# Performance work log

Measured on AMD Instinct MI355X. Metric: run time of the kernel, lower is better.

The kernel has to match this reference:

```python
import math
import jax, jax.numpy as jnp
import numpy as np

B, S, H = 8, 1024, 1024
NH = 16
HD = H // NH  # 64


def setup_inputs() -> dict:
    key = jax.random.key(0)
    k1, k2, k3, k4 = jax.random.split(key, 4)
    hidden_states = jax.random.normal(k1, (B, S, H), dtype=jnp.float32)
    attention_mask = jax.random.randint(k2, (B, 1, 1, S), 0, 2, dtype=jnp.int32)
    w_qkv = jax.random.normal(k3, (H, 3 * H), dtype=jnp.float32) * (1.0 / math.sqrt(H))
    b_qkv = jax.random.normal(k4, (3 * H,), dtype=jnp.float32) * 0.02
    return {"hidden_states": hidden_states, "attention_mask": attention_mask,
            "w_qkv": w_qkv, "b_qkv": b_qkv}


def reference(hidden_states, attention_mask, w_qkv, b_qkv):
    b, s, _ = hidden_states.shape
    # fused QKV projection: [b, s, 3H]
    qkv = jnp.einsum('bsh,hk->bsk', hidden_states, w_qkv) + b_qkv
    # view (b, s, nh, 3*hd) -> permute -> chunk last dim (per-head q|k|v layout)
    qkv = qkv.reshape(b, s, NH, 3, HD)
    qkv = jnp.transpose(qkv, (0, 2, 1, 3, 4))      # [b, nh, s, 3, hd]
    q, k, v = qkv[..., 0, :], qkv[..., 1, :], qkv[..., 2, :]
    # raw scores, then FusedScaleMaskSoftmax semantics: scale * scores, mask, fp32 softmax
    scores = jnp.einsum('bhqd,bhkd->bhqk', q, k)
    scale = math.sqrt(HD)  # module passes sqrt(head_dim) as multiplicative scale
    scores = scores.astype(jnp.float32) * scale
    mask = attention_mask != 0                     # nonzero -> masked (padding)
    scores = jnp.where(mask, jnp.float32(-10000.0), scores)
    probs = jax.nn.softmax(scores, axis=-1).astype(hidden_states.dtype)
    # dropout prob = 0 -> identity
    context = jnp.einsum('bhqk,bhkd->bhqd', probs, v)
    context = jnp.transpose(context, (0, 2, 1, 3)).reshape(b, s, NH * HD)
    return context
```

## Files before the change

### kernel.cpp

```cpp
#include <hip/hip_runtime.h>
#include <math.h>

#define Bdim 8
#define Sdim 1024
#define Hdim 1024
#define NHd 16
#define HDd 64
#define N3H 3072

#define Q_OFF   0u
#define K_OFF   16777216u
#define V_OFF   33554432u
#define WH_OFF  41943040u
#define WL_OFF  45088768u
#define AHI_OFF 0u
#define ALO_OFF 8388608u

typedef __bf16 bf16x8 __attribute__((ext_vector_type(8)));
typedef float  f32x4  __attribute__((ext_vector_type(4)));

__device__ __forceinline__ unsigned short f2bf(float x) {
  unsigned b = __builtin_bit_cast(unsigned, x);
  return (unsigned short)((b + 0x7FFFu + ((b >> 16) & 1u)) >> 16);
}
__device__ __forceinline__ float bf2f(unsigned short h) {
  unsigned b = ((unsigned)h) << 16;
  return __builtin_bit_cast(float, b);
}
__device__ __forceinline__ void split_hl(float v, unsigned short& h, unsigned short& l) {
  h = f2bf(v);
  l = f2bf(v - bf2f(h));
}
__device__ __forceinline__ void async16(void* lds, const void* g) {
  __builtin_amdgcn_global_load_lds((const __attribute__((address_space(1))) unsigned int*)g,
                                   (__attribute__((address_space(3))) unsigned int*)lds, 16, 0, 0);
}

__global__ __launch_bounds__(256) void convert_AW(
    const float* __restrict__ A, const float* __restrict__ W,
    unsigned short* __restrict__ aout, unsigned short* __restrict__ ws)
{
  __shared__ float T[64][65];
  const int tid = threadIdx.x;
  int bid = blockIdx.x;
  if (bid < 4096) {
    size_t i = ((size_t)bid * 256 + tid) * 8;
    float4 a0 = *(const float4*)&A[i];
    float4 a1 = *(const float4*)&A[i + 4];
    float av[8] = {a0.x, a0.y, a0.z, a0.w, a1.x, a1.y, a1.z, a1.w};
    unsigned short h[8], l[8];
    #pragma unroll
    for (int j = 0; j < 8; ++j) split_hl(av[j], h[j], l[j]);
    *(uint4*)&aout[AHI_OFF + i] = *(uint4*)h;
    *(uint4*)&aout[ALO_OFF + i] = *(uint4*)l;
    return;
  }
  bid -= 4096;
  const int n0 = (bid % (N3H / 64)) * 64;
  const int k0 = (bid / (N3H / 64)) * 64;
  #pragma unroll
  for (int r = 0; r < 4; ++r) {
    int k = r * 16 + (tid >> 4);
    int n = (tid & 15) * 4;
    float4 v = *(const float4*)&W[(size_t)(k0 + k) * N3H + n0 + n];
    T[k][n + 0] = v.x; T[k][n + 1] = v.y; T[k][n + 2] = v.z; T[k][n + 3] = v.w;
  }
  __syncthreads();
  int n = tid >> 2;
  int kl = (tid & 3) * 16;
  unsigned short h[16], l[16];
  #pragma unroll
  for (int i = 0; i < 16; ++i) split_hl(T[kl + i][n], h[i], l[i]);
  size_t base = (size_t)(n0 + n) * 1024 + k0 + kl;
  *(uint4*)&ws[WH_OFF + base]     = *(uint4*)&h[0];
  *(uint4*)&ws[WH_OFF + base + 8] = *(uint4*)&h[8];
  *(uint4*)&ws[WL_OFF + base]     = *(uint4*)&l[0];
  *(uint4*)&ws[WL_OFF + base + 8] = *(uint4*)&l[8];
}

__global__ __launch_bounds__(256, 2) void qkv_mfma(
    const unsigned short* __restrict__ ao,
    const unsigned short* __restrict__ ws,
    const float* __restrict__ bias,
    unsigned short* __restrict__ wso)
{
  __shared__ unsigned short sA[2][128 * 32];
  __shared__ unsigned short sB[2][128 * 32];

  const int tid  = threadIdx.x;
  const int wave = tid >> 6;
  const int lane = tid & 63;
  const int l16  = lane & 15;
  const int quad = lane >> 4;

  const int n0 = blockIdx.x * 128;
  const int m0 = blockIdx.y * 128;
  const int wm = (wave >> 1) * 64;
  const int wn = (wave & 1) * 64;

  const unsigned short* Ah = ao + AHI_OFF;
  const unsigned short* Al = ao + ALO_OFF;
  const unsigned short* Wh = ws + WH_OFF;
  const unsigned short* Wl = ws + WL_OFF;

  f32x4 acc[4][4];
  #pragma unroll
  for (int i = 0; i < 4; ++i)
    #pragma unroll
    for (int j = 0; j < 4; ++j) acc[i][j] = (f32x4){0.f, 0.f, 0.f, 0.f};

  for (int kt = 0; kt < 1024; kt += 32) {
    __syncthreads();
    #pragma unroll
    for (int r = 0; r < 2; ++r) {
      int chunk = r * 256 + tid;
      int row = chunk >> 2;
      int c8  = (chunk & 3) << 3;
      int ldsoff = (r * 256 + wave * 64) * 8;
      async16(&sA[0][ldsoff], &Ah[(size_t)(m0 + row) * 1024 + kt + c8]);
      async16(&sA[1][ldsoff], &Al[(size_t)(m0 + row) * 1024 + kt + c8]);
      async16(&sB[0][ldsoff], &Wh[(size_t)(n0 + row) * 1024 + kt + c8]);
      async16(&sB[1][ldsoff], &Wl[(size_t)(n0 + row) * 1024 + kt + c8]);
    }
    __syncthreads();

    bf16x8 af[4][2], bf[4][2];
    #pragma unroll
    for (int i = 0; i < 4; ++i) {
      int row = wm + i * 16 + l16;
      af[i][0] = *(const bf16x8*)&sA[0][row * 32 + quad * 8];
      af[i][1] = *(const bf16x8*)&sA[1][row * 32 + quad * 8];
    }
    #pragma unroll
    for (int j = 0; j < 4; ++j) {
      int row = wn + j * 16 + l16;
      bf[j][0] = *(const bf16x8*)&sB[0][row * 32 + quad * 8];
      bf[j][1] = *(const bf16x8*)&sB[1][row * 32 + quad * 8];
    }
    #pragma unroll
    for (int i = 0; i < 4; ++i)
      #pragma unroll
      for (int j = 0; j < 4; ++j) {
        acc[i][j] = __builtin_amdgcn_mfma_f32_16x16x32_bf16(af[i][0], bf[j][0], acc[i][j], 0, 0, 0);
        acc[i][j] = __builtin_amdgcn_mfma_f32_16x16x32_bf16(af[i][1], bf[j][0], acc[i][j], 0, 0, 0);
        acc[i][j] = __builtin_amdgcn_mfma_f32_16x16x32_bf16(af[i][0], bf[j][1], acc[i][j], 0, 0, 0);
      }
  }

  const int ncol0 = n0 + wn;
  const int which = (ncol0 >> 6) % 3;
  const int head  = ncol0 / 192;
  const int mrow0 = m0 + wm;
  const int bb = mrow0 >> 10;
  const int sb = mrow0 & 1023;
  const int bh = bb * NHd + head;

  float bs[4];
  #pragma unroll
  for (int j = 0; j < 4; ++j) bs[j] = bias[ncol0 + j * 16 + l16];

  if (which == 0) {
    unsigned short* dst = wso + Q_OFF + ((size_t)bh * Sdim + sb) * 128;
    #pragma unroll
    for (int i = 0; i < 4; ++i)
      #pragma unroll
      for (int j = 0; j < 4; ++j) {
        int d = j * 16 + l16;
        #pragma unroll
        for (int r = 0; r < 4; ++r) {
          int s = i * 16 + quad * 4 + r;
          unsigned short h, l;
          split_hl(acc[i][j][r] + bs[j], h, l);
          dst[(size_t)s * 128 + d]      = h;
          dst[(size_t)s * 128 + 64 + d] = l;
        }
      }
  } else if (which == 1) {
    unsigned short* dst = wso + K_OFF + (size_t)bh * 131072 + (size_t)(sb >> 6) * 8192;
    #pragma unroll
    for (int i = 0; i < 4; ++i)
      #pragma unroll
      for (int j = 0; j < 4; ++j) {
        int c = j * 16 + l16;
        #pragma unroll
        for (int r = 0; r < 4; ++r) {
          int sp = i * 16 + quad * 4 + r;
          int idx = ((((sp >> 4) * 4 + (c >> 5)) * 64 + ((c >> 3) & 3) * 16 + (sp & 15)) << 3) + (c & 7);
          unsigned short h, l;
          split_hl(acc[i][j][r] + bs[j], h, l);
          dst[idx]        = h;
          dst[idx + 1024] = l;
        }
      }
  } else {
    unsigned short* dst = wso + V_OFF + (size_t)bh * 65536 + (size_t)(sb >> 6) * 4096;
    #pragma unroll
    for (int i = 0; i < 4; ++i)
      #pragma unroll
      for (int j = 0; j < 4; ++j) {
        int dr = j * 16 + l16;
        int ky = i * 16 + quad * 4;
        int idx = ((((dr >> 4) * 2 + (ky >> 5)) * 64 + ((ky >> 3) & 3) * 16 + (dr & 15)) << 3) + (ky & 7);
        unsigned short p[4];
        #pragma unroll
        for (int r = 0; r < 4; ++r) p[r] = f2bf(acc[i][j][r] + bs[j]);
        *(uint2*)&dst[idx] = *(uint2*)p;
      }
  }
}

__global__ __launch_bounds__(256, 4) void attn_mfma(
    const unsigned short* __restrict__ qhl,
    const unsigned short* __restrict__ khl,
    const unsigned short* __restrict__ vt,
    const int* __restrict__ mask,
    float* __restrict__ out)
{
  __shared__ unsigned short Ks[8192];
  __shared__ unsigned short Vs[4096];
  __shared__ unsigned short Pw[4][1024];
  __shared__ float msks[1024];

  const int tid  = threadIdx.x;
  const int wave = tid >> 6;
  const int lane = tid & 63;
  const int l16  = lane & 15;
  const int quad = lane >> 4;

  const int bh = blockIdx.x & 127;
  const int qt = blockIdx.x >> 7;
  const int bb = bh >> 4;
  const int q0 = qt * 64;

  const unsigned short* kplane = khl + (size_t)bh * 131072;
  const unsigned short* vplane = vt  + (size_t)bh * 65536;

  {
    int4 mv = *(const int4*)&mask[bb * Sdim + tid * 4];
    msks[tid * 4 + 0] = mv.x ? 1.f : 0.f;
    msks[tid * 4 + 1] = mv.y ? 1.f : 0.f;
    msks[tid * 4 + 2] = mv.z ? 1.f : 0.f;
    msks[tid * 4 + 3] = mv.w ? 1.f : 0.f;
  }

  bf16x8 qf[4];
  {
    int row = q0 + wave * 16 + l16;
    const unsigned short* src = qhl + ((size_t)bh * Sdim + row) * 128;
    #pragma unroll
    for (int kk = 0; kk < 4; ++kk)
      qf[kk] = *(const bf16x8*)&src[kk * 32 + quad * 8];
  }

  f32x4 O[4] = {{0.f,0.f,0.f,0.f},{0.f,0.f,0.f,0.f},{0.f,0.f,0.f,0.f},{0.f,0.f,0.f,0.f}};
  float mrow[4] = {-INFINITY, -INFINITY, -INFINITY, -INFINITY};
  float lrow[4] = {0.f, 0.f, 0.f, 0.f};

  #pragma unroll 1
  for (int kt = 0; kt < 16; ++kt) {
    __syncthreads();
    {
      const unsigned short* ksrc = kplane + (size_t)kt * 8192;
      const unsigned short* vsrc = vplane + (size_t)kt * 4096;
      #pragma unroll
      for (int r = 0; r < 4; ++r)
        async16(&Ks[(r * 256 + tid) * 8], &ksrc[(size_t)(r * 256 + tid) * 8]);
      #pragma unroll
      for (int r = 0; r < 2; ++r)
        async16(&Vs[(r * 256 + tid) * 8], &vsrc[(size_t)(r * 256 + tid) * 8]);
    }
    __syncthreads();

    f32x4 sc[4];
    #pragma unroll
    for (int ns = 0; ns < 4; ++ns) {
      f32x4 c = {0.f, 0.f, 0.f, 0.f};
      bf16x8 kf0 = *(const bf16x8*)&Ks[((ns * 4 + 0) * 64 + lane) * 8];
      bf16x8 kf1 = *(const bf16x8*)&Ks[((ns * 4 + 1) * 64 + lane) * 8];
      bf16x8 kf2 = *(const bf16x8*)&Ks[((ns * 4 + 2) * 64 + lane) * 8];
      bf16x8 kf3 = *(const bf16x8*)&Ks[((ns * 4 + 3) * 64 + lane) * 8];
      c = __builtin_amdgcn_mfma_f32_16x16x32_bf16(qf[0], kf0, c, 0, 0, 0);
      c = __builtin_amdgcn_mfma_f32_16x16x32_bf16(qf[1], kf1, c, 0, 0, 0);
      c = __builtin_amdgcn_mfma_f32_16x16x32_bf16(qf[2], kf0, c, 0, 0, 0);
      c = __builtin_amdgcn_mfma_f32_16x16x32_bf16(qf[3], kf1, c, 0, 0, 0);
      c = __builtin_amdgcn_mfma_f32_16x16x32_bf16(qf[0], kf2, c, 0, 0, 0);
      c = __builtin_amdgcn_mfma_f32_16x16x32_bf16(qf[1], kf3, c, 0, 0, 0);
      sc[ns] = c;
    }

    float rmax[4] = {-INFINITY, -INFINITY, -INFINITY, -INFINITY};
    #pragma unroll
    for (int ns = 0; ns < 4; ++ns) {
      float mk = msks[kt * 64 + ns * 16 + l16];
      #pragma unroll
      for (int r = 0; r < 4; ++r) {
        float s = (mk != 0.f) ? -10000.f : sc[ns][r] * 8.f;
        sc[ns][r] = s;
        rmax[r] = fmaxf(rmax[r], s);
      }
    }
    #pragma unroll
    for (int r = 0; r < 4; ++r) {
      float v = rmax[r];
      v = fmaxf(v, __shfl_xor(v, 1, 16));
      v = fmaxf(v, __shfl_xor(v, 2, 16));
      v = fmaxf(v, __shfl_xor(v, 4, 16));
      v = fmaxf(v, __shfl_xor(v, 8, 16));
      rmax[r] = v;
    }

    float alpha[4];
    #pragma unroll
    for (int r = 0; r < 4; ++r) {
      float mn = fmaxf(mrow[r], rmax[r]);
      alpha[r] = __expf(mrow[r] - mn);
      mrow[r] = mn;
      lrow[r] *= alpha[r];
    }
    #pragma unroll
    for (int d = 0; d < 4; ++d)
      #pragma unroll
      for (int r = 0; r < 4; ++r) O[d][r] *= alpha[r];

    float rsum[4] = {0.f, 0.f, 0.f, 0.f};
    #pragma unroll
    for (int ns = 0; ns < 4; ++ns) {
      int key = ns * 16 + l16;
      int cbase = (((key >> 5) * 4 + ((key >> 3) & 3)) * 16 + quad * 4) * 8 + (key & 7);
      #pragma unroll
      for (int r = 0; r < 4; ++r) {
        float p = __expf(sc[ns][r] - mrow[r]);
        rsum[r] += p;
        Pw[wave][cbase + r * 8] = f2bf(p);
      }
    }
    #pragma unroll
    for (int r = 0; r < 4; ++r) {
      float v = rsum[r];
      v += __shfl_xor(v, 1, 16);
      v += __shfl_xor(v, 2, 16);
      v += __shfl_xor(v, 4, 16);
      v += __shfl_xor(v, 8, 16);
      lrow[r] += v;
    }

    bf16x8 pf[2];
    #pragma unroll
    for (int kk = 0; kk < 2; ++kk)
      pf[kk] = *(const bf16x8*)&Pw[wave][((kk * 4 + quad) * 16 + l16) * 8];
    #pragma unroll
    for (int d = 0; d < 4; ++d)
      #pragma unroll
      for (int kk = 0; kk < 2; ++kk) {
        bf16x8 vf = *(const bf16x8*)&Vs[((d * 2 + kk) * 64 + lane) * 8];
        O[d] = __builtin_amdgcn_mfma_f32_16x16x32_bf16(pf[kk], vf, O[d], 0, 0, 0);
      }
  }

  const int h = bh & 15;
  #pragma unroll
  for (int r = 0; r < 4; ++r) {
    float inv = 1.f / lrow[r];
    int q = q0 + wave * 16 + quad * 4 + r;
    float* dst = out + ((size_t)bb * Sdim + q) * Hdim + h * HDd;
    #pragma unroll
    for (int d = 0; d < 4; ++d)
      dst[d * 16 + l16] = O[d][r] * inv;
  }
}

extern "C" void kernel_launch(void* const* d_in, const int* in_sizes, int n_in,
                              void* d_out, int out_size, void* d_ws, size_t ws_size,
                              hipStream_t stream) {
  const float* hs   = (const float*)d_in[0];
  const int*   mask = (const int*)d_in[1];
  const float* w    = (const float*)d_in[2];
  const float* bias = (const float*)d_in[3];
  float* out = (float*)d_out;
  unsigned short* ws = (unsigned short*)d_ws;
  unsigned short* ao = (unsigned short*)d_out;

  convert_AW<<<4096 + (N3H / 64) * (1024 / 64), 256, 0, stream>>>(hs, w, ao, ws);

  qkv_mfma<<<dim3(N3H / 128, 8192 / 128), 256, 0, stream>>>(ao, ws, bias, ws);

  attn_mfma<<<Bdim * NHd * (Sdim / 64), 256, 0, stream>>>(
      ws + Q_OFF, ws + K_OFF, ws + V_OFF, mask, out);
}
```

Measured before the change: 373.9 us.

## Restructure QKV GEMM into 256x192 double-buffered tiles with swizzled LDS

```diff
diff --git a/kernel.cpp b/kernel.cpp
--- a/kernel.cpp
+++ b/kernel.cpp
@@ -78,14 +78,14 @@
   *(uint4*)&ws[WL_OFF + base + 8] = *(uint4*)&l[8];
 }
 
-__global__ __launch_bounds__(256, 2) void qkv_mfma(
+__global__ __launch_bounds__(512, 2) void qkv_mfma(
     const unsigned short* __restrict__ ao,
     const unsigned short* __restrict__ ws,
     const float* __restrict__ bias,
     unsigned short* __restrict__ wso)
 {
-  __shared__ unsigned short sA[2][128 * 32];
-  __shared__ unsigned short sB[2][128 * 32];
+  __shared__ __align__(16) unsigned short sA[2][256 * 64];
+  __shared__ __align__(16) unsigned short sB[2][192 * 64];
 
   const int tid  = threadIdx.x;
   const int wave = tid >> 6;
@@ -93,120 +93,178 @@
   const int l16  = lane & 15;
   const int quad = lane >> 4;
 
-  const int n0 = blockIdx.x * 128;
-  const int m0 = blockIdx.y * 128;
-  const int wm = (wave >> 1) * 64;
-  const int wn = (wave & 1) * 64;
-
-  const unsigned short* Ah = ao + AHI_OFF;
-  const unsigned short* Al = ao + ALO_OFF;
-  const unsigned short* Wh = ws + WH_OFF;
-  const unsigned short* Wl = ws + WL_OFF;
-
-  f32x4 acc[4][4];
+  const int bid = blockIdx.x;
+  const int swz = (bid & 7) * 64 + (bid >> 3);
+  const int bn = swz >> 5;
+  const int bm = swz & 31;
+  const int n0 = bn * 192;
+  const int m0 = bm * 256;
+
+  const int wr = wave >> 2;
+  const int wc = wave & 3;
+  const int wm = wr * 128;
+  const int wn = wc * 48;
+
+  const unsigned short* AH = ao + AHI_OFF;
+  const unsigned short* AL = ao + ALO_OFF;
+  const unsigned short* WH = ws + WH_OFF;
+  const unsigned short* WL = ws + WL_OFF;
+
+  const int rsub  = wave * 8 + (lane >> 3);
+  const int colsw = ((lane & 7) ^ (lane >> 3)) * 8;
+  const int rdswz = (l16 & 7) << 3;
+
+  f32x4 acc[8][3];
   #pragma unroll
-  for (int i = 0; i < 4; ++i)
-    #pragma unroll
-    for (int j = 0; j < 4; ++j) acc[i][j] = (f32x4){0.f, 0.f, 0.f, 0.f};
-
-  for (int kt = 0; kt < 1024; kt += 32) {
-    __syncthreads();
-    #pragma unroll
-    for (int r = 0; r < 2; ++r) {
-      int chunk = r * 256 + tid;
-      int row = chunk >> 2;
-      int c8  = (chunk & 3) << 3;
-      int ldsoff = (r * 256 + wave * 64) * 8;
-      async16(&sA[0][ldsoff], &Ah[(size_t)(m0 + row) * 1024 + kt + c8]);
-      async16(&sA[1][ldsoff], &Al[(size_t)(m0 + row) * 1024 + kt + c8]);
-      async16(&sB[0][ldsoff], &Wh[(size_t)(n0 + row) * 1024 + kt + c8]);
-      async16(&sB[1][ldsoff], &Wl[(size_t)(n0 + row) * 1024 + kt + c8]);
-    }
-    __syncthreads();
-
-    bf16x8 af[4][2], bf[4][2];
-    #pragma unroll
-    for (int i = 0; i < 4; ++i) {
-      int row = wm + i * 16 + l16;
-      af[i][0] = *(const bf16x8*)&sA[0][row * 32 + quad * 8];
-      af[i][1] = *(const bf16x8*)&sA[1][row * 32 + quad * 8];
-    }
-    #pragma unroll
-    for (int j = 0; j < 4; ++j) {
-      int row = wn + j * 16 + l16;
-      bf[j][0] = *(const bf16x8*)&sB[0][row * 32 + quad * 8];
-      bf[j][1] = *(const bf16x8*)&sB[1][row * 32 + quad * 8];
-    }
-    #pragma unroll
-    for (int i = 0; i < 4; ++i)
-      #pragma unroll
-      for (int j = 0; j < 4; ++j) {
-        acc[i][j] = __builtin_amdgcn_mfma_f32_16x16x32_bf16(af[i][0], bf[j][0], acc[i][j], 0, 0, 0);
-        acc[i][j] = __builtin_amdgcn_mfma_f32_16x16x32_bf16(af[i][1], bf[j][0], acc[i][j], 0, 0, 0);
-        acc[i][j] = __builtin_amdgcn_mfma_f32_16x16x32_bf16(af[i][0], bf[j][1], acc[i][j], 0, 0, 0);
-      }
-  }
-
-  const int ncol0 = n0 + wn;
-  const int which = (ncol0 >> 6) % 3;
-  const int head  = ncol0 / 192;
-  const int mrow0 = m0 + wm;
-  const int bb = mrow0 >> 10;
-  const int sb = mrow0 & 1023;
-  const int bh = bb * NHd + head;
-
-  float bs[4];
+  for (int i = 0; i < 8; ++i)
+    #pragma unroll
+    for (int j = 0; j < 3; ++j) acc[i][j] = (f32x4){0.f, 0.f, 0.f, 0.f};
+
+  bf16x8 af[4], bf[3];
+
+#define STAGE_A(tt, buf) do { \
+    const unsigned short* _ab = ((tt) < 16 || (tt) >= 32) ? AH : AL; \
+    const int _ko = ((tt) & 15) * 64; \
+    _Pragma("unroll") \
+    for (int q = 0; q < 4; ++q) \
+      async16(&sA[buf][q * 4096 + wave * 512], \
+              &_ab[(size_t)(m0 + q * 64 + rsub) * 1024 + _ko + colsw]); \
+  } while (0)
+
+#define STAGE_B(tt, buf) do { \
+    const unsigned short* _wb = ((tt) < 32) ? WH : WL; \
+    const int _ko = ((tt) & 15) * 64; \
+    _Pragma("unroll") \
+    for (int q = 0; q < 3; ++q) \
+      async16(&sB[buf][q * 4096 + wave * 512], \
+              &_wb[(size_t)(n0 + q * 64 + rsub) * 1024 + _ko + colsw]); \
+  } while (0)
+
+#define READ_A(h, kk) do { \
+    _Pragma("unroll") \
+    for (int i = 0; i < 4; ++i) { \
+      int row = wm + ((h) * 4 + i) * 16 + l16; \
+      af[i] = *(const bf16x8*)&sA[cur][row * 64 + ((((kk) * 32) + quad * 8) ^ rdswz)]; \
+    } \
+  } while (0)
+
+#define READ_B(kk) do { \
+    _Pragma("unroll") \
+    for (int j = 0; j < 3; ++j) { \
+      int row = wn + j * 16 + l16; \
+      bf[j] = *(const bf16x8*)&sB[cur][row * 64 + ((((kk) * 32) + quad * 8) ^ rdswz)]; \
+    } \
+  } while (0)
+
+#define MFMA12(h) do { \
+    __builtin_amdgcn_s_setprio(1); \
+    _Pragma("unroll") \
+    for (int i = 0; i < 4; ++i) \
+      _Pragma("unroll") \
+      for (int j = 0; j < 3; ++j) \
+        acc[(h) * 4 + i][j] = __builtin_amdgcn_mfma_f32_16x16x32_bf16( \
+            af[i], bf[j], acc[(h) * 4 + i][j], 0, 0, 0); \
+    __builtin_amdgcn_s_setprio(0); \
+  } while (0)
+
+#define BAR    __builtin_amdgcn_s_barrier()
+#define SCHEDB __builtin_amdgcn_sched_barrier(0)
+#define VMW0   asm volatile("s_waitcnt vmcnt(0)" ::: "memory")
+
+#define TILE_BODY(P, t_) do { \
+    const int cur = (P); \
+     \
+    READ_A(0, 0); READ_B(0); \
+    if ((t_) + 1 < 48) STAGE_A((t_) + 1, 1 - (P)); \
+    BAR; SCHEDB; MFMA12(0); BAR; \
+     \
+    READ_A(1, 0); \
+    if ((t_) + 1 < 48) STAGE_B((t_) + 1, 1 - (P)); \
+    BAR; SCHEDB; MFMA12(1); BAR; \
+     \
+    READ_A(0, 1); READ_B(1); \
+    BAR; SCHEDB; MFMA12(0); BAR; \
+     \
+    READ_A(1, 1); \
+    BAR; SCHEDB; MFMA12(1); \
+    VMW0; \
+    BAR; \
+  } while (0)
+
+  STAGE_A(0, 0); STAGE_B(0, 0);
+  VMW0;
+  BAR;
+
+  for (int t = 0; t < 48; t += 2) {
+    TILE_BODY(0, t);
+    TILE_BODY(1, t + 1);
+  }
+
+  const int bb   = m0 >> 10;
+  const int bh   = bb * NHd + bn;
+  const int srow = (m0 & 1023) + wm;
+
   #pragma unroll
-  for (int j = 0; j < 4; ++j) bs[j] = bias[ncol0 + j * 16 + l16];
-
-  if (which == 0) {
-    unsigned short* dst = wso + Q_OFF + ((size_t)bh * Sdim + sb) * 128;
-    #pragma unroll
-    for (int i = 0; i < 4; ++i)
-      #pragma unroll
-      for (int j = 0; j < 4; ++j) {
-        int d = j * 16 + l16;
+  for (int j = 0; j < 3; ++j) {
+    const int colb  = wn + j * 16;
+    const int which = colb >> 6;
+    const int d0    = colb & 63;
+    const float bsj = bias[n0 + colb + l16];
+
+    if (which == 0) {
+      unsigned short* dst = wso + Q_OFF + ((size_t)bh * Sdim) * 128;
+      #pragma unroll
+      for (int i = 0; i < 8; ++i)
         #pragma unroll
         for (int r = 0; r < 4; ++r) {
-          int s = i * 16 + quad * 4 + r;
+          int s = srow + i * 16 + quad * 4 + r;
           unsigned short h, l;
-          split_hl(acc[i][j][r] + bs[j], h, l);
-          dst[(size_t)s * 128 + d]      = h;
-          dst[(size_t)s * 128 + 64 + d] = l;
+          split_hl(acc[i][j][r] + bsj, h, l);
+          dst[(size_t)s * 128 + d0 + l16]      = h;
+          dst[(size_t)s * 128 + 64 + d0 + l16] = l;
         }
-      }
-  } else if (which == 1) {
-    unsigned short* dst = wso + K_OFF + (size_t)bh * 131072 + (size_t)(sb >> 6) * 8192;
-    #pragma unroll
-    for (int i = 0; i < 4; ++i)
-      #pragma unroll
-      for (int j = 0; j < 4; ++j) {
-        int c = j * 16 + l16;
+    } else if (which == 1) {
+      const int c = d0 + l16;
+      #pragma unroll
+      for (int i = 0; i < 8; ++i) {
+        int tile = (srow + i * 16) >> 6;
+        int spb  = (i * 16 + quad * 4) & 63;
+        unsigned short* dst = wso + K_OFF + (size_t)bh * 131072 + (size_t)tile * 8192;
         #pragma unroll
         for (int r = 0; r < 4; ++r) {
-          int sp = i * 16 + quad * 4 + r;
+          int sp = spb + r;
           int idx = ((((sp >> 4) * 4 + (c >> 5)) * 64 + ((c >> 3) & 3) * 16 + (sp & 15)) << 3) + (c & 7);
           unsigned short h, l;
-          split_hl(acc[i][j][r] + bs[j], h, l);
+          split_hl(acc[i][j][r] + bsj, h, l);
           dst[idx]        = h;
           dst[idx + 1024] = l;
         }
       }
-  } else {
-    unsigned short* dst = wso + V_OFF + (size_t)bh * 65536 + (size_t)(sb >> 6) * 4096;
-    #pragma unroll
-    for (int i = 0; i < 4; ++i)
-      #pragma unroll
-      for (int j = 0; j < 4; ++j) {
-        int dr = j * 16 + l16;
-        int ky = i * 16 + quad * 4;
+    } else {
+      const int dr = d0 + l16;
+      #pragma unroll
+      for (int i = 0; i < 8; ++i) {
+        int tile = (srow + i * 16) >> 6;
+        int ky   = (i * 16 + quad * 4) & 63;
+        unsigned short* dst = wso + V_OFF + (size_t)bh * 65536 + (size_t)tile * 4096;
         int idx = ((((dr >> 4) * 2 + (ky >> 5)) * 64 + ((ky >> 3) & 3) * 16 + (dr & 15)) << 3) + (ky & 7);
         unsigned short p[4];
         #pragma unroll
-        for (int r = 0; r < 4; ++r) p[r] = f2bf(acc[i][j][r] + bs[j]);
+        for (int r = 0; r < 4; ++r) p[r] = f2bf(acc[i][j][r] + bsj);
         *(uint2*)&dst[idx] = *(uint2*)p;
       }
-  }
+    }
+  }
+
+#undef STAGE_A
+#undef STAGE_B
+#undef READ_A
+#undef READ_B
+#undef MFMA12
+#undef BAR
+#undef SCHEDB
+#undef VMW0
+#undef TILE_BODY
 }
 
 __global__ __launch_bounds__(256, 4) void attn_mfma(
@@ -382,7 +440,7 @@
 
   convert_AW<<<4096 + (N3H / 64) * (1024 / 64), 256, 0, stream>>>(hs, w, ao, ws);
 
-  qkv_mfma<<<dim3(N3H / 128, 8192 / 128), 256, 0, stream>>>(ao, ws, bias, ws);
+  qkv_mfma<<<dim3(512), 512, 0, stream>>>(ao, ws, bias, ws);
 
   attn_mfma<<<Bdim * NHd * (Sdim / 64), 256, 0, stream>>>(
       ws + Q_OFF, ws + K_OFF, ws + V_OFF, mask, out);
```

After: 425.8 us. +13.9%, slower.

## Register-prefetch K/V tiles, skip lazy rescale, and raise MFMA priority

Applied to the files above, without the earlier changes.

```diff
diff --git a/kernel.cpp b/kernel.cpp
--- a/kernel.cpp
+++ b/kernel.cpp
@@ -209,7 +209,7 @@
   }
 }
 
-__global__ __launch_bounds__(256, 4) void attn_mfma(
+__global__ __launch_bounds__(256, 3) void attn_mfma(
     const unsigned short* __restrict__ qhl,
     const unsigned short* __restrict__ khl,
     const unsigned short* __restrict__ vt,
@@ -235,6 +235,31 @@
   const unsigned short* kplane = khl + (size_t)bh * 131072;
   const unsigned short* vplane = vt  + (size_t)bh * 65536;
 
+#define BARRIER() do { \
+    asm volatile("s_waitcnt lgkmcnt(0)" ::: "memory"); \
+    __builtin_amdgcn_sched_barrier(0); \
+    __builtin_amdgcn_s_barrier(); \
+    __builtin_amdgcn_sched_barrier(0); \
+  } while (0)
+
+  uint4 kv[6];
+#define KV_ISSUE(t_) do { \
+    const unsigned short* _ks = kplane + (size_t)(t_) * 8192; \
+    const unsigned short* _vs = vplane + (size_t)(t_) * 4096; \
+    _Pragma("unroll") \
+    for (int r = 0; r < 4; ++r) kv[r] = *(const uint4*)&_ks[(size_t)(r * 256 + tid) * 8]; \
+    _Pragma("unroll") \
+    for (int r = 0; r < 2; ++r) kv[4 + r] = *(const uint4*)&_vs[(size_t)(r * 256 + tid) * 8]; \
+  } while (0)
+#define KV_WRITE() do { \
+    _Pragma("unroll") \
+    for (int r = 0; r < 4; ++r) *(uint4*)&Ks[(r * 256 + tid) * 8] = kv[r]; \
+    _Pragma("unroll") \
+    for (int r = 0; r < 2; ++r) *(uint4*)&Vs[(r * 256 + tid) * 8] = kv[4 + r]; \
+  } while (0)
+
+  KV_ISSUE(0);
+
   {
     int4 mv = *(const int4*)&mask[bb * Sdim + tid * 4];
     msks[tid * 4 + 0] = mv.x ? 1.f : 0.f;
@@ -252,26 +277,19 @@
       qf[kk] = *(const bf16x8*)&src[kk * 32 + quad * 8];
   }
 
+  KV_WRITE();
+  KV_ISSUE(1);
+  BARRIER();
+
   f32x4 O[4] = {{0.f,0.f,0.f,0.f},{0.f,0.f,0.f,0.f},{0.f,0.f,0.f,0.f},{0.f,0.f,0.f,0.f}};
   float mrow[4] = {-INFINITY, -INFINITY, -INFINITY, -INFINITY};
   float lrow[4] = {0.f, 0.f, 0.f, 0.f};
 
   #pragma unroll 1
   for (int kt = 0; kt < 16; ++kt) {
-    __syncthreads();
-    {
-      const unsigned short* ksrc = kplane + (size_t)kt * 8192;
-      const unsigned short* vsrc = vplane + (size_t)kt * 4096;
-      #pragma unroll
-      for (int r = 0; r < 4; ++r)
-        async16(&Ks[(r * 256 + tid) * 8], &ksrc[(size_t)(r * 256 + tid) * 8]);
-      #pragma unroll
-      for (int r = 0; r < 2; ++r)
-        async16(&Vs[(r * 256 + tid) * 8], &vsrc[(size_t)(r * 256 + tid) * 8]);
-    }
-    __syncthreads();
 
     f32x4 sc[4];
+    __builtin_amdgcn_s_setprio(1);
     #pragma unroll
     for (int ns = 0; ns < 4; ++ns) {
       f32x4 c = {0.f, 0.f, 0.f, 0.f};
@@ -287,6 +305,7 @@
       c = __builtin_amdgcn_mfma_f32_16x16x32_bf16(qf[1], kf3, c, 0, 0, 0);
       sc[ns] = c;
     }
+    __builtin_amdgcn_s_setprio(0);
 
     float rmax[4] = {-INFINITY, -INFINITY, -INFINITY, -INFINITY};
     #pragma unroll
@@ -309,18 +328,22 @@
       rmax[r] = v;
     }
 
-    float alpha[4];
-    #pragma unroll
-    for (int r = 0; r < 4; ++r) {
-      float mn = fmaxf(mrow[r], rmax[r]);
-      alpha[r] = __expf(mrow[r] - mn);
-      mrow[r] = mn;
-      lrow[r] *= alpha[r];
-    }
-    #pragma unroll
-    for (int d = 0; d < 4; ++d)
-      #pragma unroll
-      for (int r = 0; r < 4; ++r) O[d][r] *= alpha[r];
+    bool nosk = !(rmax[0] <= mrow[0] + 8.f && rmax[1] <= mrow[1] + 8.f &&
+                  rmax[2] <= mrow[2] + 8.f && rmax[3] <= mrow[3] + 8.f);
+    if (__any((int)nosk)) {
+      float alpha[4];
+      #pragma unroll
+      for (int r = 0; r < 4; ++r) {
+        float mn = fmaxf(mrow[r], rmax[r]);
+        alpha[r] = __expf(mrow[r] - mn);
+        mrow[r] = mn;
+        lrow[r] *= alpha[r];
+      }
+      #pragma unroll
+      for (int d = 0; d < 4; ++d)
+        #pragma unroll
+        for (int r = 0; r < 4; ++r) O[d][r] *= alpha[r];
+    }
 
     float rsum[4] = {0.f, 0.f, 0.f, 0.f};
     #pragma unroll
@@ -348,6 +371,7 @@
     #pragma unroll
     for (int kk = 0; kk < 2; ++kk)
       pf[kk] = *(const bf16x8*)&Pw[wave][((kk * 4 + quad) * 16 + l16) * 8];
+    __builtin_amdgcn_s_setprio(1);
     #pragma unroll
     for (int d = 0; d < 4; ++d)
       #pragma unroll
@@ -355,6 +379,14 @@
         bf16x8 vf = *(const bf16x8*)&Vs[((d * 2 + kk) * 64 + lane) * 8];
         O[d] = __builtin_amdgcn_mfma_f32_16x16x32_bf16(pf[kk], vf, O[d], 0, 0, 0);
       }
+    __builtin_amdgcn_s_setprio(0);
+
+    BARRIER();
+    if (kt < 15) {
+      KV_WRITE();
+      if (kt + 2 < 16) KV_ISSUE(kt + 2);
+    }
+    BARRIER();
   }
 
   const int h = bh & 15;
@@ -367,6 +399,10 @@
     for (int d = 0; d < 4; ++d)
       dst[d * 16 + l16] = O[d][r] * inv;
   }
+
+#undef BARRIER
+#undef KV_ISSUE
+#undef KV_WRITE
 }
 
 extern "C" void kernel_launch(void* const* d_in, const int* in_sizes, int n_in,
```

New measurement: 476.0 us. 1.27x slower.
